# Kernel tuning notes

Measured on AMD Instinct MI355X. Metric: run time of the kernel, lower is better.

## Reference

```python
import jax, jax.numpy as jnp
from jax import lax
import numpy as np

DN = ('NCHW', 'OIHW', 'NCHW')

def _conv(x, w, b):
    y = lax.conv_general_dilated(x, w, (1, 1), 'VALID', dimension_numbers=DN)
    return y + b[None, :, None, None]

def _prelu(x, a):
    return jnp.where(x >= 0, x, a[None, :, None, None] * x)

def _maxpool2(x):
    # MaxPool2d(2,2,ceil_mode=True); spatial dims chosen even so VALID matches.
    return lax.reduce_window(x, -jnp.inf, lax.max, (1, 1, 2, 2), (1, 1, 2, 2), 'VALID')

def setup_inputs() -> dict:
    key = jax.random.key(0)
    ks = jax.random.split(key, 16)
    f = jnp.float32
    x = jax.random.uniform(ks[0], (16, 3, 720, 720), dtype=f) * 255.0
    def w(k, shape, fan_in):
        return jax.random.normal(k, shape, dtype=f) * (1.0 / np.sqrt(fan_in))
    return {
        'x': x,
        'conv1_w': w(ks[1], (10, 3, 3, 3), 27), 'conv1_b': jnp.zeros((10,), f),
        'prelu1_a': jnp.full((10,), 0.25, f),
        'conv2_w': w(ks[2], (16, 10, 3, 3), 90), 'conv2_b': jnp.zeros((16,), f),
        'prelu2_a': jnp.full((16,), 0.25, f),
        'conv3_w': w(ks[3], (32, 16, 3, 3), 144), 'conv3_b': jnp.zeros((32,), f),
        'prelu3_a': jnp.full((32,), 0.25, f),
        'conv41_w': w(ks[4], (2, 32, 1, 1), 32), 'conv41_b': jnp.zeros((2,), f),
        'conv42_w': w(ks[5], (4, 32, 1, 1), 32), 'conv42_b': jnp.zeros((4,), f),
    }

def reference(x, conv1_w, conv1_b, prelu1_a, conv2_w, conv2_b, prelu2_a,
              conv3_w, conv3_b, prelu3_a, conv41_w, conv41_b, conv42_w, conv42_b):
    # MTCNN pixel normalization from detect_p_net
    h = (x - 127.5) * 0.0078125
    h = _prelu(_conv(h, conv1_w, conv1_b), prelu1_a)   # [B,10,718,718]
    h = _maxpool2(h)                                   # [B,10,359,359]
    h = _prelu(_conv(h, conv2_w, conv2_b), prelu2_a)   # [B,16,357,357]
    h = _prelu(_conv(h, conv3_w, conv3_b), prelu3_a)   # [B,32,355,355]
    prob = jax.nn.softmax(_conv(h, conv41_w, conv41_b), axis=1)  # [B,2,355,355]
    reg = _conv(h, conv42_w, conv42_b)                            # [B,4,355,355]
    return (reg, prob)
```

## Files before the change

### kernel.cpp

```cpp
#include <hip/hip_runtime.h>
#include <hip/hip_bf16.h>
#include <cstddef>


#define H1 718
#define PH 359
#define H2 357
#define H3 355

#define W1R_OFF 0
#define B1R_OFF 288
#define W2R_OFF 320
#define BW3_OFF 1792
#define POOL_OFF 6400
#define C2H_OFF (POOL_OFF + (size_t)16*10*PH*PH)

typedef short bf16x8 __attribute__((ext_vector_type(8)));
typedef float f32x16 __attribute__((ext_vector_type(16)));

__global__ void repack_kernel(const float* __restrict__ w1, const float* __restrict__ b1,
                              const float* __restrict__ w2, const float* __restrict__ w3,
                              float* __restrict__ ws) {
    int t = threadIdx.x;
    const float S = 0.0078125f;
    for (int i = t; i < 270; i += blockDim.x) ws[W1R_OFF + i] = w1[i] * S;
    if (t < 10) {
        float s = 0.f;
        for (int i = 0; i < 27; i++) s += w1[t * 27 + i];
        ws[B1R_OFF + t] = b1[t] - 127.5f * S * s;
    }
    for (int i = t; i < 1440; i += blockDim.x) {
        int co = i & 15, k = i >> 4;
        ws[W2R_OFF + i] = w2[co * 90 + k];
    }
    unsigned short* bw3 = (unsigned short*)(ws + BW3_OFF);
    for (int e = t; e < 4608; e += blockDim.x) {
        int tap = e >> 9;
        int rem = e & 511;
        int l = rem >> 3, j = rem & 7;
        int kh = tap / 3, kw = tap % 3;
        int co = l & 31, ci = ((l >> 5) << 3) + j;
        float v = w3[co * 144 + ci * 9 + kh * 3 + kw];
        __hip_bfloat16 h = __float2bfloat16(v);
        bw3[e] = *(unsigned short*)&h;
    }
}

__global__ void conv1_pool_kernel(const float* __restrict__ x,
                                  const float* __restrict__ ws,
                                  const float* __restrict__ a1,
                                  float* __restrict__ pooled) {
    int pw = blockIdx.x * blockDim.x + threadIdx.x;
    int ph = blockIdx.y;
    int n  = blockIdx.z;
    if (pw >= PH) return;
    int iy = 2 * ph, ix = 2 * pw;

    float acc[10][4];
    #pragma unroll
    for (int c = 0; c < 10; c++)
        #pragma unroll
        for (int p = 0; p < 4; p++) acc[c][p] = 0.f;

    #pragma unroll
    for (int ci = 0; ci < 3; ci++) {
        const float* xp = x + (((size_t)(n * 3 + ci) * 720 + iy) * 720 + ix);
        float win[4][4];
        #pragma unroll
        for (int r = 0; r < 4; r++) {
            float2 v0 = *(const float2*)(xp + r * 720);
            float2 v1 = *(const float2*)(xp + r * 720 + 2);
            win[r][0] = v0.x; win[r][1] = v0.y; win[r][2] = v1.x; win[r][3] = v1.y;
        }
        #pragma unroll
        for (int c = 0; c < 10; c++) {
            const float* wk = ws + W1R_OFF + c * 27 + ci * 9;
            #pragma unroll
            for (int kh = 0; kh < 3; kh++)
                #pragma unroll
                for (int kw = 0; kw < 3; kw++) {
                    float wv = wk[kh * 3 + kw];
                    acc[c][0] = fmaf(win[kh    ][kw    ], wv, acc[c][0]);
                    acc[c][1] = fmaf(win[kh    ][kw + 1], wv, acc[c][1]);
                    acc[c][2] = fmaf(win[kh + 1][kw    ], wv, acc[c][2]);
                    acc[c][3] = fmaf(win[kh + 1][kw + 1], wv, acc[c][3]);
                }
        }
    }

    size_t base = ((size_t)(n * 10) * PH + ph) * PH + pw;
    const size_t cstride = (size_t)PH * PH;
    #pragma unroll
    for (int c = 0; c < 10; c++) {
        float b = ws[B1R_OFF + c], al = a1[c];
        float s0 = acc[c][0] + b, s1 = acc[c][1] + b;
        float s2 = acc[c][2] + b, s3 = acc[c][3] + b;
        s0 = s0 >= 0.f ? s0 : al * s0;
        s1 = s1 >= 0.f ? s1 : al * s1;
        s2 = s2 >= 0.f ? s2 : al * s2;
        s3 = s3 >= 0.f ? s3 : al * s3;
        pooled[base + c * cstride] = fmaxf(fmaxf(s0, s1), fmaxf(s2, s3));
    }
}

__global__ void conv2_kernel(const float* __restrict__ pooled,
                             const float* __restrict__ ws,
                             const float* __restrict__ b2,
                             const float* __restrict__ a2,
                             __hip_bfloat16* __restrict__ c2h) {
    int ow = blockIdx.x * blockDim.x + threadIdx.x;
    int oh = blockIdx.y;
    int n  = blockIdx.z;
    if (ow >= H2) return;
    const float* w2r = ws + W2R_OFF;
    float acc[16];
    #pragma unroll
    for (int co = 0; co < 16; co++) acc[co] = 0.f;
    for (int ci = 0; ci < 10; ci++) {
        const float* ip = pooled + (((size_t)(n * 10 + ci) * PH + oh) * PH + ow);
        #pragma unroll
        for (int kh = 0; kh < 3; kh++)
            #pragma unroll
            for (int kw = 0; kw < 3; kw++) {
                float v = ip[kh * PH + kw];
                const float* wp = w2r + ((ci * 3 + kh) * 3 + kw) * 16;
                #pragma unroll
                for (int co = 0; co < 16; co++) acc[co] = fmaf(v, wp[co], acc[co]);
            }
    }
    __hip_bfloat16 tmp[16];
    #pragma unroll
    for (int co = 0; co < 16; co++) {
        float v = acc[co] + b2[co];
        v = v >= 0.f ? v : a2[co] * v;
        tmp[co] = __float2bfloat16(v);
    }
    float4* dst = (float4*)(c2h + (((size_t)(n * H2 + oh) * H2 + ow) << 4));
    dst[0] = ((float4*)tmp)[0];
    dst[1] = ((float4*)tmp)[1];
}

__global__ __launch_bounds__(256, 1)
void conv3_heads_kernel(const __hip_bfloat16* __restrict__ c2h,
                        const float* __restrict__ ws,
                        const float* __restrict__ b3,
                        const float* __restrict__ a3,
                        const float* __restrict__ w41,
                        const float* __restrict__ b41,
                        const float* __restrict__ w42,
                        const float* __restrict__ b42,
                        float* __restrict__ out) {
    int wv = threadIdx.x >> 6;
    int l  = threadIdx.x & 63;
    int ow0 = blockIdx.x * 32;
    int oh0 = blockIdx.y * 8 + wv * 2;
    int n   = blockIdx.z;

    int m    = l & 31;
    int half = l >> 5;
    int choff = half << 3;

    const bf16x8* bw = (const bf16x8*)(ws + BW3_OFF);
    bf16x8 bfr[9];
    #pragma unroll
    for (int t = 0; t < 9; t++) bfr[t] = bw[t * 64 + l];

    f32x16 acc0, acc1;
    #pragma unroll
    for (int i = 0; i < 16; i++) { acc0[i] = 0.f; acc1[i] = 0.f; }

    #pragma unroll
    for (int kh = 0; kh < 3; kh++) {
        int ih0 = oh0 + kh;     if (ih0 > H2 - 1) ih0 = H2 - 1;
        int ih1 = oh0 + 1 + kh; if (ih1 > H2 - 1) ih1 = H2 - 1;
        #pragma unroll
        for (int kw = 0; kw < 3; kw++) {
            int iw = ow0 + m + kw; if (iw > H2 - 1) iw = H2 - 1;
            const bf16x8* a0p = (const bf16x8*)(c2h + ((((size_t)n * H2 + ih0) * H2 + iw) << 4) + choff);
            const bf16x8* a1p = (const bf16x8*)(c2h + ((((size_t)n * H2 + ih1) * H2 + iw) << 4) + choff);
            bf16x8 a0 = *a0p;
            bf16x8 a1 = *a1p;
            int tap = kh * 3 + kw;
            acc0 = __builtin_amdgcn_mfma_f32_32x32x16_bf16(a0, bfr[tap], acc0, 0, 0, 0);
            acc1 = __builtin_amdgcn_mfma_f32_32x32x16_bf16(a1, bfr[tap], acc1, 0, 0, 0);
        }
    }

    __shared__ float hbuf[4][64 * 33];
    float* hb = hbuf[wv];
    float bb = b3[m], aa = a3[m];
    #pragma unroll
    for (int t = 0; t < 2; t++) {
        #pragma unroll
        for (int r = 0; r < 16; r++) {
            int mprime = (r & 3) + ((r >> 2) << 3) + (half << 2);
            float v = (t ? acc1[r] : acc0[r]) + bb;
            v = v >= 0.f ? v : aa * v;
            hb[(t * 32 + mprime) * 33 + m] = v;
        }
    }
    __syncthreads();

    int poh = oh0 + (l >> 5);
    int pow_ = ow0 + (l & 31);
    float h[32];
    #pragma unroll
    for (int c = 0; c < 32; c++) h[c] = hb[l * 33 + c];

    float l0 = b41[0], l1 = b41[1];
    float r0 = b42[0], r1 = b42[1], r2 = b42[2], r3 = b42[3];
    #pragma unroll
    for (int c = 0; c < 32; c++) {
        float hv = h[c];
        l0 = fmaf(hv, w41[c],      l0);
        l1 = fmaf(hv, w41[32 + c], l1);
        r0 = fmaf(hv, w42[c],      r0);
        r1 = fmaf(hv, w42[32 + c], r1);
        r2 = fmaf(hv, w42[64 + c], r2);
        r3 = fmaf(hv, w42[96 + c], r3);
    }
    float mx  = fmaxf(l0, l1);
    float e0 = __expf(l0 - mx), e1 = __expf(l1 - mx);
    float inv = 1.0f / (e0 + e1);

    if (poh < H3 && pow_ < H3) {
        const size_t sp = (size_t)H3 * H3;
        size_t pos = (size_t)poh * H3 + pow_;
        float* reg  = out;
        float* prob = out + (size_t)16 * 4 * sp;
        reg[((size_t)(n * 4 + 0)) * sp + pos] = r0;
        reg[((size_t)(n * 4 + 1)) * sp + pos] = r1;
        reg[((size_t)(n * 4 + 2)) * sp + pos] = r2;
        reg[((size_t)(n * 4 + 3)) * sp + pos] = r3;
        prob[((size_t)(n * 2 + 0)) * sp + pos] = e0 * inv;
        prob[((size_t)(n * 2 + 1)) * sp + pos] = e1 * inv;
    }
}

extern "C" void kernel_launch(void* const* d_in, const int* in_sizes, int n_in,
                              void* d_out, int out_size, void* d_ws, size_t ws_size,
                              hipStream_t stream) {
    const float* x   = (const float*)d_in[0];
    const float* w1  = (const float*)d_in[1];
    const float* b1  = (const float*)d_in[2];
    const float* a1  = (const float*)d_in[3];
    const float* w2  = (const float*)d_in[4];
    const float* b2  = (const float*)d_in[5];
    const float* a2  = (const float*)d_in[6];
    const float* w3  = (const float*)d_in[7];
    const float* b3  = (const float*)d_in[8];
    const float* a3  = (const float*)d_in[9];
    const float* w41 = (const float*)d_in[10];
    const float* b41 = (const float*)d_in[11];
    const float* w42 = (const float*)d_in[12];
    const float* b42 = (const float*)d_in[13];
    float* out = (float*)d_out;
    float* ws  = (float*)d_ws;

    float* pooled        = ws + POOL_OFF;
    __hip_bfloat16* c2h  = (__hip_bfloat16*)(ws + C2H_OFF);

    repack_kernel<<<1, 256, 0, stream>>>(w1, b1, w2, w3, ws);

    {
        dim3 grid((PH + 127) / 128, PH, 16);
        conv1_pool_kernel<<<grid, 128, 0, stream>>>(x, ws, a1, pooled);
    }
    {
        dim3 grid((H2 + 127) / 128, H2, 16);
        conv2_kernel<<<grid, 128, 0, stream>>>(pooled, ws, b2, a2, c2h);
    }
    {
        dim3 grid((H3 + 31) / 32, (H3 + 7) / 8, 16);
        conv3_heads_kernel<<<grid, 256, 0, stream>>>(c2h, ws, b3, a3,
                                                     w41, b41, w42, b42, out);
    }
}
```

Before: 346.9 us.

## Run conv2 on bf16 MFMA with a channel-last bf16 pooled buffer

```diff
diff --git a/kernel.cpp b/kernel.cpp
--- a/kernel.cpp
+++ b/kernel.cpp
@@ -10,13 +10,15 @@
 
 #define W1R_OFF 0
 #define B1R_OFF 288
-#define W2R_OFF 320
-#define BW3_OFF 1792
-#define POOL_OFF 6400
-#define C2H_OFF (POOL_OFF + (size_t)16*10*PH*PH)
+#define AW2_OFF 320
+#define BW3_OFF 1600
+#define P16_OFF 4096
+#define C2H_OFF 16500864
 
 typedef short bf16x8 __attribute__((ext_vector_type(8)));
+typedef float f32x4  __attribute__((ext_vector_type(4)));
 typedef float f32x16 __attribute__((ext_vector_type(16)));
+typedef unsigned short ushort4v __attribute__((ext_vector_type(4)));
 
 __global__ void repack_kernel(const float* __restrict__ w1, const float* __restrict__ b1,
                               const float* __restrict__ w2, const float* __restrict__ w3,
@@ -29,9 +31,17 @@
         for (int i = 0; i < 27; i++) s += w1[t * 27 + i];
         ws[B1R_OFF + t] = b1[t] - 127.5f * S * s;
     }
-    for (int i = t; i < 1440; i += blockDim.x) {
-        int co = i & 15, k = i >> 4;
-        ws[W2R_OFF + i] = w2[co * 90 + k];
+    unsigned short* aw2 = (unsigned short*)(ws + AW2_OFF);
+    for (int e = t; e < 2560; e += blockDim.x) {
+        int s = e >> 9;
+        int rem = e & 511;
+        int l = rem >> 3, j = rem & 7;
+        int q = l >> 4, co = l & 15;
+        int tap = 2 * s + (q >> 1);
+        int ci  = ((q & 1) << 3) + j;
+        float v = (tap < 9 && ci < 10) ? w2[co * 90 + ci * 9 + tap] : 0.f;
+        __hip_bfloat16 h = __float2bfloat16(v);
+        aw2[e] = *(unsigned short*)&h;
     }
     unsigned short* bw3 = (unsigned short*)(ws + BW3_OFF);
     for (int e = t; e < 4608; e += blockDim.x) {
@@ -49,7 +59,7 @@
 __global__ void conv1_pool_kernel(const float* __restrict__ x,
                                   const float* __restrict__ ws,
                                   const float* __restrict__ a1,
-                                  float* __restrict__ pooled) {
+                                  __hip_bfloat16* __restrict__ p16) {
     int pw = blockIdx.x * blockDim.x + threadIdx.x;
     int ph = blockIdx.y;
     int n  = blockIdx.z;
@@ -88,8 +98,7 @@
         }
     }
 
-    size_t base = ((size_t)(n * 10) * PH + ph) * PH + pw;
-    const size_t cstride = (size_t)PH * PH;
+    __hip_bfloat16 o[16];
     #pragma unroll
     for (int c = 0; c < 10; c++) {
         float b = ws[B1R_OFF + c], al = a1[c];
@@ -99,45 +108,83 @@
         s1 = s1 >= 0.f ? s1 : al * s1;
         s2 = s2 >= 0.f ? s2 : al * s2;
         s3 = s3 >= 0.f ? s3 : al * s3;
-        pooled[base + c * cstride] = fmaxf(fmaxf(s0, s1), fmaxf(s2, s3));
-    }
-}
-
-__global__ void conv2_kernel(const float* __restrict__ pooled,
-                             const float* __restrict__ ws,
-                             const float* __restrict__ b2,
-                             const float* __restrict__ a2,
-                             __hip_bfloat16* __restrict__ c2h) {
-    int ow = blockIdx.x * blockDim.x + threadIdx.x;
-    int oh = blockIdx.y;
-    int n  = blockIdx.z;
-    if (ow >= H2) return;
-    const float* w2r = ws + W2R_OFF;
-    float acc[16];
-    #pragma unroll
-    for (int co = 0; co < 16; co++) acc[co] = 0.f;
-    for (int ci = 0; ci < 10; ci++) {
-        const float* ip = pooled + (((size_t)(n * 10 + ci) * PH + oh) * PH + ow);
-        #pragma unroll
-        for (int kh = 0; kh < 3; kh++)
+        o[c] = __float2bfloat16(fmaxf(fmaxf(s0, s1), fmaxf(s2, s3)));
+    }
+    #pragma unroll
+    for (int c = 10; c < 16; c++) o[c] = __float2bfloat16(0.f);
+
+    float4* dst = (float4*)(p16 + (((size_t)n * PH + ph) * PH + pw) * 16);
+    dst[0] = ((float4*)o)[0];
+    dst[1] = ((float4*)o)[1];
+}
+
+__global__ __launch_bounds__(256)
+void conv2_mfma_kernel(const __hip_bfloat16* __restrict__ p16,
+                       const float* __restrict__ ws,
+                       const float* __restrict__ b2,
+                       const float* __restrict__ a2,
+                       __hip_bfloat16* __restrict__ c2h) {
+    int wv = threadIdx.x >> 6;
+    int l  = threadIdx.x & 63;
+    int oh  = blockIdx.y * 4 + wv;
+    int ow0 = blockIdx.x * 64;
+    int n   = blockIdx.z;
+    if (oh >= H2) return;
+
+    int pxl = l & 15;
+    int q   = l >> 4;
+    int taph = q >> 1;
+    int choff = (q & 1) << 3;
+
+    const bf16x8* aw = (const bf16x8*)(ws + AW2_OFF);
+    bf16x8 afr[5];
+    #pragma unroll
+    for (int s = 0; s < 5; s++) afr[s] = aw[s * 64 + l];
+
+    bf16x8 zf;
+    #pragma unroll
+    for (int j = 0; j < 8; j++) zf[j] = 0;
+
+    f32x4 acc[4];
+    #pragma unroll
+    for (int t = 0; t < 4; t++)
+        #pragma unroll
+        for (int i = 0; i < 4; i++) acc[t][i] = 0.f;
+
+    #pragma unroll
+    for (int s = 0; s < 5; s++) {
+        int tap = 2 * s + taph;
+        bool real = (tap < 9);
+        int kh = tap / 3, kw = tap - kh * 3;
+        int ih = oh + kh; if (ih > PH - 1) ih = PH - 1;
+        #pragma unroll
+        for (int t = 0; t < 4; t++) {
+            int iw = ow0 + t * 16 + pxl + kw; if (iw > PH - 1) iw = PH - 1;
+            const bf16x8* bp = (const bf16x8*)(p16 + (((size_t)n * PH + ih) * PH + iw) * 16 + choff);
+            bf16x8 b = real ? *bp : zf;
+            acc[t] = __builtin_amdgcn_mfma_f32_16x16x32_bf16(afr[s], b, acc[t], 0, 0, 0);
+        }
+    }
+
+    float bb[4], aa[4];
+    #pragma unroll
+    for (int r = 0; r < 4; r++) { bb[r] = b2[q * 4 + r]; aa[r] = a2[q * 4 + r]; }
+
+    #pragma unroll
+    for (int t = 0; t < 4; t++) {
+        int px = ow0 + t * 16 + pxl;
+        if (px < H2) {
+            ushort4v pk;
             #pragma unroll
-            for (int kw = 0; kw < 3; kw++) {
-                float v = ip[kh * PH + kw];
-                const float* wp = w2r + ((ci * 3 + kh) * 3 + kw) * 16;
-                #pragma unroll
-                for (int co = 0; co < 16; co++) acc[co] = fmaf(v, wp[co], acc[co]);
+            for (int r = 0; r < 4; r++) {
+                float v = acc[t][r] + bb[r];
+                v = v >= 0.f ? v : aa[r] * v;
+                __hip_bfloat16 h = __float2bfloat16(v);
+                pk[r] = *(unsigned short*)&h;
             }
-    }
-    __hip_bfloat16 tmp[16];
-    #pragma unroll
-    for (int co = 0; co < 16; co++) {
-        float v = acc[co] + b2[co];
-        v = v >= 0.f ? v : a2[co] * v;
-        tmp[co] = __float2bfloat16(v);
-    }
-    float4* dst = (float4*)(c2h + (((size_t)(n * H2 + oh) * H2 + ow) << 4));
-    dst[0] = ((float4*)tmp)[0];
-    dst[1] = ((float4*)tmp)[1];
+            *(ushort4v*)(c2h + (((size_t)n * H2 + oh) * H2 + px) * 16 + q * 4) = pk;
+        }
+    }
 }
 
 __global__ __launch_bounds__(256, 1)
@@ -257,18 +304,18 @@
     float* out = (float*)d_out;
     float* ws  = (float*)d_ws;
 
-    float* pooled        = ws + POOL_OFF;
-    __hip_bfloat16* c2h  = (__hip_bfloat16*)(ws + C2H_OFF);
+    __hip_bfloat16* p16 = (__hip_bfloat16*)(ws + P16_OFF);
+    __hip_bfloat16* c2h = (__hip_bfloat16*)(ws + C2H_OFF);
 
     repack_kernel<<<1, 256, 0, stream>>>(w1, b1, w2, w3, ws);
 
     {
         dim3 grid((PH + 127) / 128, PH, 16);
-        conv1_pool_kernel<<<grid, 128, 0, stream>>>(x, ws, a1, pooled);
+        conv1_pool_kernel<<<grid, 128, 0, stream>>>(x, ws, a1, p16);
     }
     {
-        dim3 grid((H2 + 127) / 128, H2, 16);
-        conv2_kernel<<<grid, 128, 0, stream>>>(pooled, ws, b2, a2, c2h);
+        dim3 grid((H2 + 63) / 64, (H2 + 3) / 4, 16);
+        conv2_mfma_kernel<<<grid, 256, 0, stream>>>(p16, ws, b2, a2, c2h);
     }
     {
         dim3 grid((H3 + 31) / 32, (H3 + 7) / 8, 16);
```

Result: faster. 316.6 us (-8.7%).
